# Kernel optimization log

Measured on AMD Instinct MI355X. Metric: run time of the kernel, lower is better.

The kernel has to match this reference:

```python
import math
import jax, jax.numpy as jnp
import numpy as np

D_MODEL = 1024
NUM_HEADS = 16
D_K = D_MODEL // NUM_HEADS
THETA = 10000.0
MAX_SEQ_LEN = 2048
BATCH = 2
SEQ = 2048


def build_rope_matrices(theta, d_k, max_seq_len):
    # Faithful to the torch buffer: per-position d_k x d_k tridiagonal rotation matrix.
    k = jnp.arange(d_k)
    inv_freq = jnp.power(theta, -2.0 * (k // 2) / d_k)  # [d_k]
    pos = jnp.arange(max_seq_len, dtype=jnp.float32)[:, None]  # [S,1]
    ang = pos * inv_freq[None, :]  # [S, d_k]
    cos_v = jnp.cos(ang)  # main diagonal
    sin_v = jnp.sin(jnp.where(k % 2 == 0, ang, 0.0))[:, :-1]  # sub/super diagonal, len d_k-1

    def mk(c, s):
        return jnp.diag(c) + jnp.diag(s, -1) + jnp.diag(-s, 1)

    return jax.vmap(mk)(cos_v, sin_v)  # [max_seq_len, d_k, d_k]


def setup_inputs() -> dict:
    key = jax.random.key(0)
    k1, k2, k3 = jax.random.split(key, 3)
    x = jax.random.normal(k1, (BATCH, SEQ, D_MODEL), dtype=jnp.float32)
    token_positions = jnp.arange(SEQ, dtype=jnp.int64 if jax.config.jax_enable_x64 else jnp.int32)
    # trunc_normal init approximated by scaled normal (same distribution family / scale)
    std_attn = 2.0 / (D_MODEL + 3 * D_MODEL)
    std_out = 2.0 / (D_MODEL + D_MODEL)
    W_attn = jax.random.normal(k2, (3 * NUM_HEADS * D_K, D_MODEL), dtype=jnp.float32) * std_attn
    W_out = jax.random.normal(k3, (D_MODEL, NUM_HEADS * D_K), dtype=jnp.float32) * std_out
    rope = build_rope_matrices(THETA, D_K, MAX_SEQ_LEN)
    return {"x": x, "W_attn": W_attn, "W_out": W_out, "rope": rope,
            "token_positions": token_positions}


def reference(x, W_attn, W_out, rope, token_positions):
    B, S, _ = x.shape
    # QKV projection: '... d_in, d_out d_in -> ... d_out'
    proj = jnp.einsum('bsd,ed->bse', x, W_attn)  # [B,S,3*H*dk]
    proj = proj.reshape(B, S, 3, NUM_HEADS, D_K)
    proj = jnp.transpose(proj, (2, 0, 3, 1, 4))  # [3,B,H,S,dk]
    Q, K, V = proj[0], proj[1], proj[2]
    # RoPE via per-position matrix multiply (faithful to module)
    R = rope[token_positions]  # [S, dk, dk]
    Q = jnp.einsum('sij,bhsj->bhsi', R, Q)
    K = jnp.einsum('sij,bhsj->bhsi', R, K)
    # naive causal attention with full score matrix (faithful)
    scores = jnp.einsum('bhnd,bhmd->bhnm', Q, K) / math.sqrt(D_K)
    causal = jnp.tril(jnp.ones((S, S), dtype=bool))
    scores = jnp.where(causal, scores, -jnp.inf)
    attn = jax.nn.softmax(scores, axis=-1)
    attended = jnp.einsum('bhnm,bhmd->bhnd', attn, V)  # [B,H,S,dk]
    concat = jnp.transpose(attended, (0, 2, 1, 3)).reshape(B, S, NUM_HEADS * D_K)
    return jnp.einsum('bse,de->bsd', concat, W_out)
```

## Files before the change

### kernel.cpp

```cpp
#include <hip/hip_runtime.h>
#include <math.h>

#define B_SZ 2
#define SEQ 2048
#define DMODEL 1024
#define NH 16
#define DK 64
#define NQKV 3072
#define M_ROWS 4096

#define NEG_BIG (-3.0e38f)
#define SCL 0.18033688011112042f

typedef short short8 __attribute__((ext_vector_type(8)));
typedef float v4f __attribute__((ext_vector_type(4)));
typedef unsigned short ushort_t;

__device__ inline ushort_t f2bf(float f) {
    unsigned u = __float_as_uint(f);
    u += 0x7fffu + ((u >> 16) & 1u);
    return (ushort_t)(u >> 16);
}

__device__ __forceinline__ unsigned cvt_pk_bf16(float lo, float hi) {
    unsigned r;
    asm("v_cvt_pk_bf16_f32 %0, %1, %2" : "=v"(r) : "v"(lo), "v"(hi));
    return r;
}
__device__ __forceinline__ void permlane32_swap(unsigned &a, unsigned &b) {
    asm("v_permlane32_swap_b32 %0, %1" : "+v"(a), "+v"(b));
}
__device__ __forceinline__ void permlane16_swap(unsigned &a, unsigned &b) {
    asm("v_permlane16_swap_b32 %0, %1" : "+v"(a), "+v"(b));
}

__device__ __forceinline__ void gl_lds16(const ushort_t* g, ushort_t* l) {
    __builtin_amdgcn_global_load_lds(
        (const __attribute__((address_space(1))) unsigned int*)g,
        (__attribute__((address_space(3))) unsigned int*)l, 16, 0, 0);
}

__global__ __launch_bounds__(256) void prep_kernel(
    const float* __restrict__ x, const float* __restrict__ Wa,
    const float* __restrict__ Wo, const float* __restrict__ rope,
    ushort_t* __restrict__ xb, ushort_t* __restrict__ Wab, ushort_t* __restrict__ Wob,
    float* __restrict__ cosT, float* __restrict__ sinT)
{
    const int bid = blockIdx.x;
    if (bid < 8192) {
        const float* src; ushort_t* dst; int i;
        if (bid < 4096)      { src = x;  dst = xb;  i = bid * 256 + threadIdx.x; }
        else if (bid < 7168) { src = Wa; dst = Wab; i = (bid - 4096) * 256 + threadIdx.x; }
        else                 { src = Wo; dst = Wob; i = (bid - 7168) * 256 + threadIdx.x; }
        float4 v = reinterpret_cast<const float4*>(src)[i];
        ushort4 r;
        r.x = f2bf(v.x); r.y = f2bf(v.y); r.z = f2bf(v.z); r.w = f2bf(v.w);
        reinterpret_cast<ushort4*>(dst)[i] = r;
    } else {
        const int i = (bid - 8192) * 256 + threadIdx.x;
        const int p = i >> 6, d = i & 63;
        const float* Rp = rope + (size_t)p * 4096;
        const float c = Rp[d * 64 + d];
        const float s = Rp[(d | 1) * 64 + (d & ~1)];
        cosT[i] = c;
        sinT[i] = (d & 1) ? s : -s;
    }
}

#define ES_STRIDE 136

#define QKV_STAGE(bofs, k0s)                                                   \
    _Pragma("unroll")                                                          \
    for (int j = 0; j < 4; ++j)                                                \
        gl_lds16(&Wab[(size_t)(e0 + srow[j]) * DMODEL + (k0s) + skc[j]],       \
                 &qkv_smem[(bofs) + (tid + 256 * j) * 8]);                     \
    _Pragma("unroll")                                                          \
    for (int j = 4; j < 8; ++j)                                                \
        gl_lds16(&xb[(size_t)(m0 + srow[j]) * DMODEL + (k0s) + skc[j]],        \
                 &qkv_smem[(bofs) + (tid + 256 * j) * 8]);

__global__ __launch_bounds__(256) void qkv_mfma_kernel(
    const ushort_t* __restrict__ xb,
    const ushort_t* __restrict__ Wab,
    const float* __restrict__ cosT, const float* __restrict__ sinT,
    const int* __restrict__ tpos,
    ushort_t* __restrict__ Qb, ushort_t* __restrict__ Kb, ushort_t* __restrict__ Vtb)
{
    __shared__ ushort_t qkv_smem[32768];
    ushort_t* Es = qkv_smem;

    const int tid = threadIdx.x;
    const int w = tid >> 6, lane = tid & 63;
    const int lm = lane & 15, g = lane >> 4;
    const int wm = (w >> 1) * 64, wn = (w & 1) * 64;

    const int lid = blockIdx.y * 24 + blockIdx.x;
    const int swz = (lid & 7) * 96 + (lid >> 3);
    const int e0 = (swz % 24) * 128, m0 = (swz / 24) * 128;

    int srow[8], skc[8];
#pragma unroll
    for (int j = 0; j < 8; ++j) {
        const int c = tid + 256 * j;
        const int cm = c & 1023;
        const int row = cm >> 3, pp = cm & 7;
        srow[j] = row;
        skc[j] = (pp ^ (row & 7)) * 8;
    }

    v4f acc[4][4] = {};

    QKV_STAGE(0, 0);

    for (int t = 0; t < 16; ++t) {
        const int bofs = (t & 1) << 14;
        if (t < 15) {
            const int nofs = ((t + 1) & 1) << 14;
            QKV_STAGE(nofs, (t + 1) * 64);
            __builtin_amdgcn_sched_barrier(0);
            asm volatile("s_waitcnt vmcnt(8)" ::: "memory");
        } else {
            __builtin_amdgcn_sched_barrier(0);
            asm volatile("s_waitcnt vmcnt(0)" ::: "memory");
        }
        __builtin_amdgcn_s_barrier();
        __builtin_amdgcn_sched_barrier(0);

        __builtin_amdgcn_s_setprio(1);
#pragma unroll
        for (int kb = 0; kb < 2; ++kb) {
            short8 af[4], bfr[4];
#pragma unroll
            for (int mf = 0; mf < 4; ++mf) {
                const int r = wm + mf * 16 + lm;
                af[mf] = *reinterpret_cast<const short8*>(
                    &qkv_smem[bofs + (r * 8 + ((kb * 4 + g) ^ (r & 7))) * 8]);
            }
#pragma unroll
            for (int nf = 0; nf < 4; ++nf) {
                const int r = wn + nf * 16 + lm;
                bfr[nf] = *reinterpret_cast<const short8*>(
                    &qkv_smem[bofs + 8192 + (r * 8 + ((kb * 4 + g) ^ (r & 7))) * 8]);
            }
#pragma unroll
            for (int mf = 0; mf < 4; ++mf)
#pragma unroll
                for (int nf = 0; nf < 4; ++nf)
                    acc[mf][nf] = __builtin_amdgcn_mfma_f32_16x16x32_bf16(af[mf], bfr[nf], acc[mf][nf], 0, 0, 0);
        }
        __builtin_amdgcn_s_setprio(0);

        __builtin_amdgcn_sched_barrier(0);
        __builtin_amdgcn_s_barrier();
        __builtin_amdgcn_sched_barrier(0);
    }

    __syncthreads();

    const int which = e0 >> 10;
    const int h0 = (e0 & 1023) >> 6;
    const int bb = m0 >> 11, s0 = m0 & 2047;

    if (which < 2) {
        ushort_t* buf = (which == 0) ? Qb : Kb;
        const float qs = (which == 0) ? SCL : 1.0f;
#pragma unroll
        for (int mf = 0; mf < 4; ++mf) {
            const int ebase = wm + mf * 16 + g * 4;
            const int d0 = (e0 + ebase) & 63;
#pragma unroll
            for (int nf = 0; nf < 4; ++nf) {
                const int sloc = wn + nf * 16 + lm;
                float v[4] = {acc[mf][nf][0], acc[mf][nf][1], acc[mf][nf][2], acc[mf][nf][3]};
                const int p = tpos[s0 + sloc];
                const float4 c4 = *reinterpret_cast<const float4*>(&cosT[p * 64 + d0]);
                const float4 s4 = *reinterpret_cast<const float4*>(&sinT[p * 64 + d0]);
                const float r0 = (c4.x * v[0] + s4.x * v[1]) * qs;
                const float r1 = (c4.y * v[1] + s4.y * v[0]) * qs;
                const float r2 = (c4.z * v[2] + s4.z * v[3]) * qs;
                const float r3 = (c4.w * v[3] + s4.w * v[2]) * qs;
                uint2 pp;
                pp.x = (unsigned)f2bf(r0) | ((unsigned)f2bf(r1) << 16);
                pp.y = (unsigned)f2bf(r2) | ((unsigned)f2bf(r3) << 16);
                *reinterpret_cast<uint2*>(&Es[sloc * ES_STRIDE + ebase]) = pp;
            }
        }
        __syncthreads();
#pragma unroll
        for (int hh = 0; hh < 2; ++hh) {
            ushort_t* dst = buf + (((size_t)bb * NH + h0 + hh) * SEQ + s0) * DK;
#pragma unroll
            for (int t = 0; t < 4; ++t) {
                const int o = (t * 256 + tid) * 8;
                const int sloc = o >> 6, d = o & 63;
                const short8 vv = *reinterpret_cast<const short8*>(&Es[sloc * ES_STRIDE + hh * 64 + d]);
                *reinterpret_cast<short8*>(&dst[o]) = vv;
            }
        }
    } else {
#pragma unroll
        for (int mf = 0; mf < 4; ++mf) {
            const int ebase = wm + mf * 16 + g * 4;
#pragma unroll
            for (int nf = 0; nf < 4; ++nf) {
                const int sloc = wn + nf * 16 + lm;
                Es[(ebase + 0) * ES_STRIDE + sloc] = f2bf(acc[mf][nf][0]);
                Es[(ebase + 1) * ES_STRIDE + sloc] = f2bf(acc[mf][nf][1]);
                Es[(ebase + 2) * ES_STRIDE + sloc] = f2bf(acc[mf][nf][2]);
                Es[(ebase + 3) * ES_STRIDE + sloc] = f2bf(acc[mf][nf][3]);
            }
        }
        __syncthreads();
#pragma unroll
        for (int t = 0; t < 8; ++t) {
            const int c = t * 256 + tid;
            const int hh = c >> 10, cm = c & 1023;
            const int d = cm >> 4, s8c = (cm & 15) * 8;
            const short8 vv = *reinterpret_cast<const short8*>(&Es[(hh * 64 + d) * ES_STRIDE + s8c]);
            ushort_t* dst = Vtb + ((size_t)bb * NH + h0 + hh) * SEQ * DK + (size_t)d * SEQ + s0 + s8c;
            *reinterpret_cast<short8*>(dst) = vv;
        }
    }
}

#define ATTN_STEP(QF0, QF1, QROW, LACC, OACC, DIAG, C0)                           \
    {                                                                             \
        v4f sacc[4] = {};                                                         \
        _Pragma("unroll")                                                         \
        for (int nf = 0; nf < 4; ++nf) {                                          \
            sacc[nf] = __builtin_amdgcn_mfma_f32_16x16x32_bf16(kf[nf][0], QF0, sacc[nf], 0, 0, 0); \
            sacc[nf] = __builtin_amdgcn_mfma_f32_16x16x32_bf16(kf[nf][1], QF1, sacc[nf], 0, 0, 0); \
        }                                                                         \
        if (DIAG) {                                                               \
            _Pragma("unroll")                                                     \
            for (int nf = 0; nf < 4; ++nf)                                        \
                _Pragma("unroll")                                                 \
                for (int reg = 0; reg < 4; ++reg) {                               \
                    const int kv = (C0) + nf * 16 + g * 4 + reg;                  \
                    if (kv > (QROW)) sacc[nf][reg] = NEG_BIG;                     \
                }                                                                 \
        }                                                                         \
        unsigned pk0[8];                                                          \
        _Pragma("unroll")                                                         \
        for (int nf = 0; nf < 4; ++nf) {                                          \
            pk0[nf * 2]     = cvt_pk_bf16(exp2f(sacc[nf][0]), exp2f(sacc[nf][1])); \
            pk0[nf * 2 + 1] = cvt_pk_bf16(exp2f(sacc[nf][2]), exp2f(sacc[nf][3])); \
        }                                                                         \
        _Pragma("unroll")                                                         \
        for (int kc = 0; kc < 2; ++kc) {                                          \
            unsigned x0 = pk0[kc * 4 + 0], y0 = pk0[kc * 4 + 2];                  \
            unsigned x1 = pk0[kc * 4 + 1], y1 = pk0[kc * 4 + 3];                  \
            permlane32_swap(x0, y0); permlane16_swap(x0, y0);                     \
            permlane32_swap(x1, y1); permlane16_swap(x1, y1);                     \
            union { unsigned u[4]; short8 s; } pu;                                \
            pu.u[0] = x0; pu.u[1] = x1; pu.u[2] = y0; pu.u[3] = y1;               \
            const short8 pf = pu.s;                                               \
            LACC = __builtin_amdgcn_mfma_f32_16x16x32_bf16(ones8, pf, LACC, 0, 0, 0); \
            _Pragma("unroll")                                                     \
            for (int df = 0; df < 4; ++df)                                        \
                OACC[df] = __builtin_amdgcn_mfma_f32_16x16x32_bf16(vf[df][kc], pf, OACC[df], 0, 0, 0); \
        }                                                                         \
    }

__global__ __launch_bounds__(256, 2) void attn_mfma_kernel(
    const ushort_t* __restrict__ Qb, const ushort_t* __restrict__ Kb,
    const ushort_t* __restrict__ Vtb, ushort_t* __restrict__ attb)
{
    __shared__ ushort_t Ks[2][64][72];
    __shared__ ushort_t Vs[2][64][72];

    const int tid = threadIdx.x;
    const int w = tid >> 6, lane = tid & 63;
    const int lm = lane & 15, g = lane >> 4, lk8 = g * 8;

    const int u = blockIdx.x;
    const int h = blockIdx.y, b = blockIdx.z;
    const size_t ho = ((size_t)b * NH + h) * SEQ * DK;
    const ushort_t* Qh = Qb + ho;
    const ushort_t* Kh = Kb + ho;
    const ushort_t* Vth = Vtb + ho;

    const int rr0 = tid >> 3, cc80 = (tid & 7) * 8;
    const int rr1 = (tid + 256) >> 3, cc81 = ((tid + 256) & 7) * 8;

    const int it1 = u, it2 = 31 - u;
    const int qrowA = it1 * 64 + w * 16 + lm;
    const int qrowB = it2 * 64 + w * 16 + lm;

    const short8 qa0 = *reinterpret_cast<const short8*>(&Qh[(size_t)qrowA * DK + lk8]);
    const short8 qa1 = *reinterpret_cast<const short8*>(&Qh[(size_t)qrowA * DK + 32 + lk8]);
    const short8 qb0 = *reinterpret_cast<const short8*>(&Qh[(size_t)qrowB * DK + lk8]);
    const short8 qb1 = *reinterpret_cast<const short8*>(&Qh[(size_t)qrowB * DK + 32 + lk8]);

    const short8 ones8 = {16256, 16256, 16256, 16256, 16256, 16256, 16256, 16256};

    v4f laccA = {}, laccB = {};
    v4f OA[4] = {}, OB[4] = {};

    short8 kreg[2], vreg[2];
    kreg[0] = *reinterpret_cast<const short8*>(&Kh[(size_t)rr0 * DK + cc80]);
    kreg[1] = *reinterpret_cast<const short8*>(&Kh[(size_t)rr1 * DK + cc81]);
    vreg[0] = *reinterpret_cast<const short8*>(&Vth[(size_t)rr0 * SEQ + cc80]);
    vreg[1] = *reinterpret_cast<const short8*>(&Vth[(size_t)rr1 * SEQ + cc81]);

    for (int jt = 0; jt <= it2; ++jt) {
        const int c0 = jt * 64;
        const int bufi = jt & 1;
        ushort_t (*Ksb)[72] = Ks[bufi];
        ushort_t (*Vsb)[72] = Vs[bufi];

        *reinterpret_cast<short8*>(&Ksb[rr0][cc80]) = kreg[0];
        *reinterpret_cast<short8*>(&Ksb[rr1][cc81]) = kreg[1];
        *reinterpret_cast<short8*>(&Vsb[rr0][cc80]) = vreg[0];
        *reinterpret_cast<short8*>(&Vsb[rr1][cc81]) = vreg[1];

        if (jt < it2) {
            const int c0n = c0 + 64;
            kreg[0] = *reinterpret_cast<const short8*>(&Kh[(size_t)(c0n + rr0) * DK + cc80]);
            kreg[1] = *reinterpret_cast<const short8*>(&Kh[(size_t)(c0n + rr1) * DK + cc81]);
            vreg[0] = *reinterpret_cast<const short8*>(&Vth[(size_t)rr0 * SEQ + c0n + cc80]);
            vreg[1] = *reinterpret_cast<const short8*>(&Vth[(size_t)rr1 * SEQ + c0n + cc81]);
        }

        __syncthreads();

        short8 kf[4][2], vf[4][2];
#pragma unroll
        for (int nf = 0; nf < 4; ++nf) {
            kf[nf][0] = *reinterpret_cast<const short8*>(&Ksb[nf * 16 + lm][lk8]);
            kf[nf][1] = *reinterpret_cast<const short8*>(&Ksb[nf * 16 + lm][32 + lk8]);
        }
#pragma unroll
        for (int df = 0; df < 4; ++df) {
            vf[df][0] = *reinterpret_cast<const short8*>(&Vsb[df * 16 + lm][lk8]);
            vf[df][1] = *reinterpret_cast<const short8*>(&Vsb[df * 16 + lm][32 + lk8]);
        }

        ATTN_STEP(qb0, qb1, qrowB, laccB, OB, (jt == it2), c0)
        if (jt <= it1) {
            ATTN_STEP(qa0, qa1, qrowA, laccA, OA, (jt == it1), c0)
        }
    }

    {
        const float inv = 1.0f / laccA[0];
#pragma unroll
        for (int df = 0; df < 4; ++df) {
            uint2 st;
            st.x = cvt_pk_bf16(OA[df][0] * inv, OA[df][1] * inv);
            st.y = cvt_pk_bf16(OA[df][2] * inv, OA[df][3] * inv);
            *reinterpret_cast<uint2*>(
                &attb[((size_t)b * SEQ + qrowA) * DMODEL + h * DK + df * 16 + g * 4]) = st;
        }
    }
    {
        const float inv = 1.0f / laccB[0];
#pragma unroll
        for (int df = 0; df < 4; ++df) {
            uint2 st;
            st.x = cvt_pk_bf16(OB[df][0] * inv, OB[df][1] * inv);
            st.y = cvt_pk_bf16(OB[df][2] * inv, OB[df][3] * inv);
            *reinterpret_cast<uint2*>(
                &attb[((size_t)b * SEQ + qrowB) * DMODEL + h * DK + df * 16 + g * 4]) = st;
        }
    }
}

#define OUT_STAGE(bofs, k0s)                                                   \
    _Pragma("unroll")                                                          \
    for (int j = 0; j < 4; ++j)                                                \
        gl_lds16(&attb[(size_t)(m0 + srow[j]) * DMODEL + (k0s) + skc[j]],      \
                 &smem[(bofs) + (tid + 256 * j) * 8]);                         \
    _Pragma("unroll")                                                          \
    for (int j = 4; j < 8; ++j)                                                \
        gl_lds16(&Wob[(size_t)(n0 + srow[j]) * DMODEL + (k0s) + skc[j]],       \
                 &smem[(bofs) + (tid + 256 * j) * 8]);

__global__ __launch_bounds__(256) void out_mfma_kernel(
    const ushort_t* __restrict__ attb,
    const ushort_t* __restrict__ Wob,
    float* __restrict__ out)
{
    __shared__ ushort_t smem[32768];

    const int tid = threadIdx.x;
    const int w = tid >> 6, lane = tid & 63;
    const int lm = lane & 15, g = lane >> 4;
    const int wm = (w >> 1) * 64, wn = (w & 1) * 64;

    const int lid = blockIdx.y * 8 + blockIdx.x;
    const int swz = (lid & 7) * 32 + (lid >> 3);
    const int m0 = (swz >> 3) * 128, n0 = (swz & 7) * 128;

    int srow[8], skc[8];
#pragma unroll
    for (int j = 0; j < 8; ++j) {
        const int c = tid + 256 * j;
        const int cm = c & 1023;
        const int row = cm >> 3, pp = cm & 7;
        srow[j] = row;
        skc[j] = (pp ^ (row & 7)) * 8;
    }

    v4f acc[4][4] = {};

    OUT_STAGE(0, 0);

    for (int t = 0; t < 16; ++t) {
        const int bofs = (t & 1) << 14;
        if (t < 15) {
            const int nofs = ((t + 1) & 1) << 14;
            OUT_STAGE(nofs, (t + 1) * 64);
            __builtin_amdgcn_sched_barrier(0);
            asm volatile("s_waitcnt vmcnt(8)" ::: "memory");
        } else {
            __builtin_amdgcn_sched_barrier(0);
            asm volatile("s_waitcnt vmcnt(0)" ::: "memory");
        }
        __builtin_amdgcn_s_barrier();
        __builtin_amdgcn_sched_barrier(0);

        __builtin_amdgcn_s_setprio(1);
#pragma unroll
        for (int kb = 0; kb < 2; ++kb) {
            short8 af[4], bfr[4];
#pragma unroll
            for (int mf = 0; mf < 4; ++mf) {
                const int r = wm + mf * 16 + lm;
                af[mf] = *reinterpret_cast<const short8*>(
                    &smem[bofs + (r * 8 + ((kb * 4 + g) ^ (r & 7))) * 8]);
            }
#pragma unroll
            for (int nf = 0; nf < 4; ++nf) {
                const int r = wn + nf * 16 + lm;
                bfr[nf] = *reinterpret_cast<const short8*>(
                    &smem[bofs + 8192 + (r * 8 + ((kb * 4 + g) ^ (r & 7))) * 8]);
            }
#pragma unroll
            for (int mf = 0; mf < 4; ++mf)
#pragma unroll
                for (int nf = 0; nf < 4; ++nf)
                    acc[mf][nf] = __builtin_amdgcn_mfma_f32_16x16x32_bf16(af[mf], bfr[nf], acc[mf][nf], 0, 0, 0);
        }
        __builtin_amdgcn_s_setprio(0);

        __builtin_amdgcn_sched_barrier(0);
        __builtin_amdgcn_s_barrier();
        __builtin_amdgcn_sched_barrier(0);
    }

#pragma unroll
    for (int mf = 0; mf < 4; ++mf)
#pragma unroll
        for (int reg = 0; reg < 4; ++reg) {
            const int m = m0 + wm + mf * 16 + g * 4 + reg;
#pragma unroll
            for (int nf = 0; nf < 4; ++nf) {
                const int n = n0 + wn + nf * 16 + lm;
                out[(size_t)m * DMODEL + n] = acc[mf][nf][reg];
            }
        }
}

extern "C" void kernel_launch(void* const* d_in, const int* in_sizes, int n_in,
                              void* d_out, int out_size, void* d_ws, size_t ws_size,
                              hipStream_t stream) {
    (void)in_sizes; (void)n_in; (void)out_size; (void)ws_size;

    const float* x    = (const float*)d_in[0];
    const float* Wa   = (const float*)d_in[1];
    const float* Wo   = (const float*)d_in[2];
    const float* rope = (const float*)d_in[3];
    const int*   tp   = (const int*)d_in[4];
    float* out = (float*)d_out;

    char* ws = (char*)d_ws;
    ushort_t* xb   = (ushort_t*)(ws);
    ushort_t* Wab  = (ushort_t*)(ws + (8u << 20));
    ushort_t* Wob  = (ushort_t*)(ws + (14u << 20));
    float*    cosT = (float*)   (ws + (16u << 20));
    float*    sinT = (float*)   (ws + (16u << 20) + (512u << 10));
    ushort_t* Qb   = (ushort_t*)(ws + (17u << 20));
    ushort_t* Kb   = (ushort_t*)(ws + (25u << 20));
    ushort_t* Vtb  = (ushort_t*)(ws + (33u << 20));
    ushort_t* attb = (ushort_t*)(ws + (41u << 20));

    dim3 blk(256);
    prep_kernel<<<dim3(8704), blk, 0, stream>>>(x, Wa, Wo, rope, xb, Wab, Wob, cosT, sinT);

    qkv_mfma_kernel<<<dim3(NQKV / 128, M_ROWS / 128), blk, 0, stream>>>(
        xb, Wab, cosT, sinT, tp, Qb, Kb, Vtb);
    attn_mfma_kernel<<<dim3(16, NH, B_SZ), blk, 0, stream>>>(Qb, Kb, Vtb, attb);
    out_mfma_kernel<<<dim3(DMODEL / 128, M_ROWS / 128), blk, 0, stream>>>(attb, Wob, out);
}
```

Measured before the change: 207.8 us.

## Enlarge QKV GEMM tile to 256x256 with 8 waves and phased quarter-tile pipeline

The QKV projection kernel moves from 128x128 tiles with 4 waves to 256x256 tiles with 8 waves. The K-loop is split into four phases that each stage one quarter of the next tile's operands, with finer vmcnt waits, while MFMA work runs on the current buffer. The goal is more operand reuse per LDS load and fewer global loads per FLOP. The cost is a grid of only 192 blocks, lower occupancy from 128KB LDS and larger accumulators, and an epilogue split into two halves to fit the staging buffer.

```diff
diff --git a/kernel.cpp b/kernel.cpp
--- a/kernel.cpp
+++ b/kernel.cpp
@@ -67,95 +67,116 @@
     }
 }
 
-#define ES_STRIDE 136
-
-#define QKV_STAGE(bofs, k0s)                                                   \
-    _Pragma("unroll")                                                          \
-    for (int j = 0; j < 4; ++j)                                                \
-        gl_lds16(&Wab[(size_t)(e0 + srow[j]) * DMODEL + (k0s) + skc[j]],       \
-                 &qkv_smem[(bofs) + (tid + 256 * j) * 8]);                     \
-    _Pragma("unroll")                                                          \
-    for (int j = 4; j < 8; ++j)                                                \
-        gl_lds16(&xb[(size_t)(m0 + srow[j]) * DMODEL + (k0s) + skc[j]],        \
-                 &qkv_smem[(bofs) + (tid + 256 * j) * 8]);
-
-__global__ __launch_bounds__(256) void qkv_mfma_kernel(
+__global__ __launch_bounds__(512, 2) void qkv_mfma_kernel(
     const ushort_t* __restrict__ xb,
     const ushort_t* __restrict__ Wab,
     const float* __restrict__ cosT, const float* __restrict__ sinT,
     const int* __restrict__ tpos,
     ushort_t* __restrict__ Qb, ushort_t* __restrict__ Kb, ushort_t* __restrict__ Vtb)
 {
-    __shared__ ushort_t qkv_smem[32768];
+    __shared__ ushort_t qkv_smem[65536];
     ushort_t* Es = qkv_smem;
 
     const int tid = threadIdx.x;
-    const int w = tid >> 6, lane = tid & 63;
+    const int wid = tid >> 6, lane = tid & 63;
     const int lm = lane & 15, g = lane >> 4;
-    const int wm = (w >> 1) * 64, wn = (w & 1) * 64;
-
-    const int lid = blockIdx.y * 24 + blockIdx.x;
-    const int swz = (lid & 7) * 96 + (lid >> 3);
-    const int e0 = (swz % 24) * 128, m0 = (swz / 24) * 128;
-
-    int srow[8], skc[8];
-#pragma unroll
-    for (int j = 0; j < 8; ++j) {
-        const int c = tid + 256 * j;
-        const int cm = c & 1023;
-        const int row = cm >> 3, pp = cm & 7;
-        srow[j] = row;
-        skc[j] = (pp ^ (row & 7)) * 8;
-    }
-
-    v4f acc[4][4] = {};
-
-    QKV_STAGE(0, 0);
+    const int wr = wid >> 2, wc = wid & 3;
+
+    const int lid = blockIdx.y * 12 + blockIdx.x;
+    const int swz = (lid & 7) * 24 + (lid >> 3);
+    const int e0 = (swz % 12) * 256, m0 = (swz / 12) * 256;
+
+    int koff[2], partsA[2], partsB[2];
+#pragma unroll
+    for (int j = 0; j < 2; ++j) {
+        const int c = tid + 512 * j;
+        const int rA = c >> 3, pp = c & 7;
+        koff[j] = (pp ^ (rA & 7)) * 8;
+        partsA[j] = ((rA >> 6) << 7) + (rA & 63);
+        partsB[j] = ((rA >> 5) << 6) + (rA & 31);
+    }
+
+    auto stage = [&](int t, int kind) {
+        const int base = ((t & 1) << 15) + (kind << 13);
+        const int k0 = t << 6;
+        if (kind < 2) {
+#pragma unroll
+            for (int j = 0; j < 2; ++j)
+                gl_lds16(&Wab[(size_t)(e0 + partsA[j] + kind * 64) * DMODEL + k0 + koff[j]],
+                         &qkv_smem[base + (tid + 512 * j) * 8]);
+        } else {
+#pragma unroll
+            for (int j = 0; j < 2; ++j)
+                gl_lds16(&xb[(size_t)(m0 + partsB[j] + (kind - 2) * 32) * DMODEL + k0 + koff[j]],
+                         &qkv_smem[base + (tid + 512 * j) * 8]);
+        }
+    };
+
+    v4f acc[8][4] = {};
+    short8 afr[2][4][2];
+    short8 bfr[2][2];
+
+    stage(0, 0); stage(0, 2); stage(0, 1); stage(0, 3);
 
     for (int t = 0; t < 16; ++t) {
-        const int bofs = (t & 1) << 14;
-        if (t < 15) {
-            const int nofs = ((t + 1) & 1) << 14;
-            QKV_STAGE(nofs, (t + 1) * 64);
+        const int dbase = (t & 1) << 15;
+#pragma unroll
+        for (int ph = 0; ph < 4; ++ph) {
+            const int korder = (ph == 0) ? 0 : (ph == 1) ? 2 : (ph == 2) ? 1 : 3;
+            if (t < 15) stage(t + 1, korder);
             __builtin_amdgcn_sched_barrier(0);
-            asm volatile("s_waitcnt vmcnt(8)" ::: "memory");
-        } else {
+            if (t < 15) {
+                asm volatile("s_waitcnt vmcnt(6)" ::: "memory");
+            } else {
+                if (ph == 0)      asm volatile("s_waitcnt vmcnt(4)" ::: "memory");
+                else if (ph == 1) asm volatile("s_waitcnt vmcnt(2)" ::: "memory");
+                else if (ph == 2) asm volatile("s_waitcnt vmcnt(0)" ::: "memory");
+            }
+            __builtin_amdgcn_s_barrier();
             __builtin_amdgcn_sched_barrier(0);
-            asm volatile("s_waitcnt vmcnt(0)" ::: "memory");
-        }
-        __builtin_amdgcn_s_barrier();
-        __builtin_amdgcn_sched_barrier(0);
-
-        __builtin_amdgcn_s_setprio(1);
-#pragma unroll
-        for (int kb = 0; kb < 2; ++kb) {
-            short8 af[4], bfr[4];
-#pragma unroll
-            for (int mf = 0; mf < 4; ++mf) {
-                const int r = wm + mf * 16 + lm;
-                af[mf] = *reinterpret_cast<const short8*>(
-                    &qkv_smem[bofs + (r * 8 + ((kb * 4 + g) ^ (r & 7))) * 8]);
-            }
-#pragma unroll
-            for (int nf = 0; nf < 4; ++nf) {
-                const int r = wn + nf * 16 + lm;
-                bfr[nf] = *reinterpret_cast<const short8*>(
-                    &qkv_smem[bofs + 8192 + (r * 8 + ((kb * 4 + g) ^ (r & 7))) * 8]);
-            }
-#pragma unroll
-            for (int mf = 0; mf < 4; ++mf)
-#pragma unroll
-                for (int nf = 0; nf < 4; ++nf)
-                    acc[mf][nf] = __builtin_amdgcn_mfma_f32_16x16x32_bf16(af[mf], bfr[nf], acc[mf][nf], 0, 0, 0);
-        }
-        __builtin_amdgcn_s_setprio(0);
-
-        __builtin_amdgcn_sched_barrier(0);
-        __builtin_amdgcn_s_barrier();
-        __builtin_amdgcn_sched_barrier(0);
-    }
-
-    __syncthreads();
+
+            const int eh = (ph == 1 || ph == 2) ? 1 : 0;
+            const int sh = (ph >= 2) ? 1 : 0;
+
+            if (ph == 0 || ph == 1) {
+#pragma unroll
+                for (int i = 0; i < 4; ++i) {
+                    const int r = wr * 64 + i * 16 + lm;
+#pragma unroll
+                    for (int kb = 0; kb < 2; ++kb)
+                        afr[eh][i][kb] = *reinterpret_cast<const short8*>(
+                            &qkv_smem[dbase + eh * 8192 +
+                                      (r * 8 + ((kb * 4 + g) ^ (r & 7))) * 8]);
+                }
+            }
+            if (ph == 0 || ph == 2) {
+#pragma unroll
+                for (int j = 0; j < 2; ++j) {
+                    const int r = wc * 32 + j * 16 + lm;
+#pragma unroll
+                    for (int kb = 0; kb < 2; ++kb)
+                        bfr[j][kb] = *reinterpret_cast<const short8*>(
+                            &qkv_smem[dbase + 16384 + sh * 8192 +
+                                      (r * 8 + ((kb * 4 + g) ^ (r & 7))) * 8]);
+                }
+            }
+
+            __builtin_amdgcn_s_setprio(1);
+#pragma unroll
+            for (int i = 0; i < 4; ++i)
+#pragma unroll
+                for (int j = 0; j < 2; ++j)
+#pragma unroll
+                    for (int kb = 0; kb < 2; ++kb)
+                        acc[eh * 4 + i][sh * 2 + j] = __builtin_amdgcn_mfma_f32_16x16x32_bf16(
+                            afr[eh][i][kb], bfr[j][kb], acc[eh * 4 + i][sh * 2 + j], 0, 0, 0);
+            __builtin_amdgcn_s_setprio(0);
+
+            __builtin_amdgcn_sched_barrier(0);
+            __builtin_amdgcn_s_barrier();
+            __builtin_amdgcn_sched_barrier(0);
+        }
+    }
 
     const int which = e0 >> 10;
     const int h0 = (e0 & 1023) >> 6;
@@ -165,60 +186,74 @@
         ushort_t* buf = (which == 0) ? Qb : Kb;
         const float qs = (which == 0) ? SCL : 1.0f;
 #pragma unroll
-        for (int mf = 0; mf < 4; ++mf) {
-            const int ebase = wm + mf * 16 + g * 4;
-            const int d0 = (e0 + ebase) & 63;
-#pragma unroll
-            for (int nf = 0; nf < 4; ++nf) {
-                const int sloc = wn + nf * 16 + lm;
-                float v[4] = {acc[mf][nf][0], acc[mf][nf][1], acc[mf][nf][2], acc[mf][nf][3]};
-                const int p = tpos[s0 + sloc];
-                const float4 c4 = *reinterpret_cast<const float4*>(&cosT[p * 64 + d0]);
-                const float4 s4 = *reinterpret_cast<const float4*>(&sinT[p * 64 + d0]);
-                const float r0 = (c4.x * v[0] + s4.x * v[1]) * qs;
-                const float r1 = (c4.y * v[1] + s4.y * v[0]) * qs;
-                const float r2 = (c4.z * v[2] + s4.z * v[3]) * qs;
-                const float r3 = (c4.w * v[3] + s4.w * v[2]) * qs;
-                uint2 pp;
-                pp.x = (unsigned)f2bf(r0) | ((unsigned)f2bf(r1) << 16);
-                pp.y = (unsigned)f2bf(r2) | ((unsigned)f2bf(r3) << 16);
-                *reinterpret_cast<uint2*>(&Es[sloc * ES_STRIDE + ebase]) = pp;
-            }
-        }
-        __syncthreads();
-#pragma unroll
-        for (int hh = 0; hh < 2; ++hh) {
-            ushort_t* dst = buf + (((size_t)bb * NH + h0 + hh) * SEQ + s0) * DK;
-#pragma unroll
-            for (int t = 0; t < 4; ++t) {
-                const int o = (t * 256 + tid) * 8;
-                const int sloc = o >> 6, d = o & 63;
-                const short8 vv = *reinterpret_cast<const short8*>(&Es[sloc * ES_STRIDE + hh * 64 + d]);
-                *reinterpret_cast<short8*>(&dst[o]) = vv;
+        for (int half = 0; half < 2; ++half) {
+            __syncthreads();
+            if ((wc >> 1) == half) {
+#pragma unroll
+                for (int mf = 0; mf < 8; ++mf) {
+                    const int ebase = wr * 128 + (mf >> 2) * 64 + (mf & 3) * 16 + g * 4;
+                    const int d0 = ebase & 63;
+#pragma unroll
+                    for (int nf = 0; nf < 4; ++nf) {
+                        const int slocg = wc * 64 + (nf >> 1) * 32 + (nf & 1) * 16 + lm;
+                        const int sloc = slocg & 127;
+                        float v[4] = {acc[mf][nf][0], acc[mf][nf][1], acc[mf][nf][2], acc[mf][nf][3]};
+                        const int p = tpos[s0 + slocg];
+                        const float4 c4 = *reinterpret_cast<const float4*>(&cosT[p * 64 + d0]);
+                        const float4 s4 = *reinterpret_cast<const float4*>(&sinT[p * 64 + d0]);
+                        const float r0 = (c4.x * v[0] + s4.x * v[1]) * qs;
+                        const float r1 = (c4.y * v[1] + s4.y * v[0]) * qs;
+                        const float r2 = (c4.z * v[2] + s4.z * v[3]) * qs;
+                        const float r3 = (c4.w * v[3] + s4.w * v[2]) * qs;
+                        uint2 pp;
+                        pp.x = cvt_pk_bf16(r0, r1);
+                        pp.y = cvt_pk_bf16(r2, r3);
+                        *reinterpret_cast<uint2*>(&Es[sloc * 264 + ebase]) = pp;
+                    }
+                }
+            }
+            __syncthreads();
+#pragma unroll
+            for (int r = 0; r < 8; ++r) {
+                const int idx = r * 512 + tid;
+                const int sloc = idx >> 5, ec = (idx & 31) * 8;
+                const int hh = ec >> 6, d = ec & 63;
+                const short8 vv = *reinterpret_cast<const short8*>(&Es[sloc * 264 + ec]);
+                ushort_t* dst = buf + (((size_t)bb * NH + h0 + hh) * SEQ +
+                                       (s0 + half * 128 + sloc)) * DK + d;
+                *reinterpret_cast<short8*>(dst) = vv;
             }
         }
     } else {
 #pragma unroll
-        for (int mf = 0; mf < 4; ++mf) {
-            const int ebase = wm + mf * 16 + g * 4;
-#pragma unroll
-            for (int nf = 0; nf < 4; ++nf) {
-                const int sloc = wn + nf * 16 + lm;
-                Es[(ebase + 0) * ES_STRIDE + sloc] = f2bf(acc[mf][nf][0]);
-                Es[(ebase + 1) * ES_STRIDE + sloc] = f2bf(acc[mf][nf][1]);
-                Es[(ebase + 2) * ES_STRIDE + sloc] = f2bf(acc[mf][nf][2]);
-                Es[(ebase + 3) * ES_STRIDE + sloc] = f2bf(acc[mf][nf][3]);
-            }
-        }
-        __syncthreads();
-#pragma unroll
-        for (int t = 0; t < 8; ++t) {
-            const int c = t * 256 + tid;
-            const int hh = c >> 10, cm = c & 1023;
-            const int d = cm >> 4, s8c = (cm & 15) * 8;
-            const short8 vv = *reinterpret_cast<const short8*>(&Es[(hh * 64 + d) * ES_STRIDE + s8c]);
-            ushort_t* dst = Vtb + ((size_t)bb * NH + h0 + hh) * SEQ * DK + (size_t)d * SEQ + s0 + s8c;
-            *reinterpret_cast<short8*>(dst) = vv;
+        for (int half = 0; half < 2; ++half) {
+            __syncthreads();
+            if ((wc >> 1) == half) {
+#pragma unroll
+                for (int mf = 0; mf < 8; ++mf) {
+                    const int ebase = wr * 128 + (mf >> 2) * 64 + (mf & 3) * 16 + g * 4;
+#pragma unroll
+                    for (int nf = 0; nf < 4; ++nf) {
+                        const int slocg = wc * 64 + (nf >> 1) * 32 + (nf & 1) * 16 + lm;
+                        const int sloc = slocg & 127;
+                        Es[(ebase + 0) * 136 + sloc] = f2bf(acc[mf][nf][0]);
+                        Es[(ebase + 1) * 136 + sloc] = f2bf(acc[mf][nf][1]);
+                        Es[(ebase + 2) * 136 + sloc] = f2bf(acc[mf][nf][2]);
+                        Es[(ebase + 3) * 136 + sloc] = f2bf(acc[mf][nf][3]);
+                    }
+                }
+            }
+            __syncthreads();
+#pragma unroll
+            for (int r = 0; r < 8; ++r) {
+                const int idx = r * 512 + tid;
+                const int erow = idx >> 4, sc8 = (idx & 15) * 8;
+                const int hh = erow >> 6, d = erow & 63;
+                const short8 vv = *reinterpret_cast<const short8*>(&Es[erow * 136 + sc8]);
+                ushort_t* dst = Vtb + (((size_t)bb * NH + h0 + hh) * DK + d) * SEQ +
+                                s0 + half * 128 + sc8;
+                *reinterpret_cast<short8*>(dst) = vv;
+            }
         }
     }
 }
@@ -488,7 +523,7 @@
     dim3 blk(256);
     prep_kernel<<<dim3(8704), blk, 0, stream>>>(x, Wa, Wo, rope, xb, Wab, Wob, cosT, sinT);
 
-    qkv_mfma_kernel<<<dim3(NQKV / 128, M_ROWS / 128), blk, 0, stream>>>(
+    qkv_mfma_kernel<<<dim3(NQKV / 256, M_ROWS / 256), dim3(512), 0, stream>>>(
         xb, Wab, cosT, sinT, tp, Qb, Kb, Vtb);
     attn_mfma_kernel<<<dim3(16, NH, B_SZ), blk, 0, stream>>>(Qb, Kb, Vtb, attb);
     out_mfma_kernel<<<dim3(DMODEL / 128, M_ROWS / 128), blk, 0, stream>>>(attb, Wob, out);
```

New measurement: 203.9 us. Within noise of the previous version (-1.9%).
